# Kernel optimization log

Measured on AMD Instinct MI355X. Metric: run time of the kernel, lower is better.

Reference implementation:

```python
import jax, jax.numpy as jnp
import numpy as np

N, E, G = 50000, 600000, 500          # nodes, edges, graphs in batch
IN_NODE, HID, EDGE = 92, 64, 41       # CGCNN default feature dims
NCONV, PRED, NOUT = 3, 128, 1
Z_DIM = 2 * HID + EDGE                # 169: cat(src_x, dst_x, edge_attr)
BN_EPS = 1e-5


def setup_inputs() -> dict:
    key = jax.random.key(0)
    ks = jax.random.split(key, 14)
    f32 = jnp.float32
    return {
        "x": jax.random.normal(ks[0], (N, IN_NODE), f32),
        "edge_attr": jax.random.normal(ks[1], (E, EDGE), f32),
        "src": jax.random.randint(ks[2], (E,), 0, N),
        "dst": jax.random.randint(ks[3], (E,), 0, N),
        "graph_idx": jnp.sort(jax.random.randint(ks[4], (N,), 0, G)),
        "n_graphs": G,
        "W_embed": jax.random.normal(ks[5], (IN_NODE, HID), f32) / np.sqrt(IN_NODE),
        "b_embed": jnp.zeros((HID,), f32),
        "W_sig": jax.random.normal(ks[6], (NCONV, Z_DIM, HID), f32) / np.sqrt(Z_DIM),
        "b_sig": jnp.zeros((NCONV, HID), f32),
        "W_sp": jax.random.normal(ks[7], (NCONV, Z_DIM, HID), f32) / np.sqrt(Z_DIM),
        "b_sp": jnp.zeros((NCONV, HID), f32),
        "bn_gamma": jnp.ones((NCONV, HID), f32),
        "bn_beta": jnp.zeros((NCONV, HID), f32),
        "W_fc": jax.random.normal(ks[8], (HID, PRED), f32) / np.sqrt(HID),
        "b_fc": jnp.zeros((PRED,), f32),
        "W_out": jax.random.normal(ks[9], (PRED, NOUT), f32) / np.sqrt(PRED),
        "b_out": jnp.zeros((NOUT,), f32),
    }


def reference(x, edge_attr, src, dst, graph_idx, n_graphs,
              W_embed, b_embed, W_sig, b_sig, W_sp, b_sp,
              bn_gamma, bn_beta, W_fc, b_fc, W_out, b_out):
    # node embedding to hidden dim
    h = x @ W_embed + b_embed                                   # [N, HID]
    n_nodes = h.shape[0]
    for i in range(W_sig.shape[0]):
        # per-edge features: gather src/dst node feats + edge feats
        z = jnp.concatenate([h[src], h[dst], edge_attr], axis=1)  # [E, Z_DIM]
        gated = jax.nn.sigmoid(z @ W_sig[i] + b_sig[i])           # [E, HID]
        msg = jax.nn.softplus(z @ W_sp[i] + b_sp[i])              # [E, HID]
        # scatter-sum gated messages into destination node mailboxes
        agg = jax.ops.segment_sum(gated * msg, dst, num_segments=n_nodes)
        h = h + agg                                               # residual
        # batch norm over nodes (training-mode batch stats, biased var)
        mean = h.mean(axis=0)
        var = h.var(axis=0)
        h = (h - mean) * jax.lax.rsqrt(var + BN_EPS) * bn_gamma[i] + bn_beta[i]
    # sum-pool nodes per graph, then dense readout
    graph_feat = jax.ops.segment_sum(h, graph_idx, num_segments=n_graphs)  # [G, HID]
    graph_feat = graph_feat @ W_fc + b_fc                                  # [G, PRED]
    return graph_feat @ W_out + b_out                                      # [G, NOUT]
```

## Files before the change

### kernel.cpp

```cpp
#include <hip/hip_runtime.h>

#define N_NODES 50000
#define N_EDGES 600000
#define N_GRAPHS 500
#define IN_F 92
#define HID 64
#define EDGE_F 41
#define ZDIM 169
#define PRED 128
#define BN_EPS 1e-5f
#define SCAN_BLOCKS 196
#define ROW_U32 24
#define LOG2E 1.4426950408889634f
#define LN2   0.6931471805599453f

typedef unsigned int u32;
typedef _Float16 f16;
typedef _Float16 f16x2 __attribute__((ext_vector_type(2)));
typedef _Float16 f16x8 __attribute__((ext_vector_type(8)));
typedef float f32x4 __attribute__((ext_vector_type(4)));

__device__ __forceinline__ u32 f2bf(float f) {
    u32 u = __float_as_uint(f);
    return (u + 0x7fffu + ((u >> 16) & 1u)) >> 16;
}

__device__ __forceinline__ int lbound(const int* __restrict__ a, int nelem, int val) {
    int lo = 0, hi = nelem;
    while (lo < hi) {
        int m = (lo + hi) >> 1;
        if (a[m] < val) lo = m + 1; else hi = m;
    }
    return lo;
}

__global__ void k_zeroAll(int* __restrict__ ip, int n1, float* __restrict__ fp, int n2) {
    int i = blockIdx.x * 256 + threadIdx.x;
    if (i < n1) ip[i] = 0;
    else if (i - n1 < n2) fp[i - n1] = 0.f;
}

__global__ void k_hist(const int* __restrict__ dst, int* __restrict__ deg) {
    int e = blockIdx.x * 256 + threadIdx.x;
    if (e < N_EDGES) atomicAdd(&deg[dst[e]], 1);
}

__global__ __launch_bounds__(256) void k_scanA(const int* __restrict__ deg,
                                               int* __restrict__ partial) {
    __shared__ int s[256];
    int i = blockIdx.x * 256 + threadIdx.x;
    s[threadIdx.x] = (i < N_NODES) ? deg[i] : 0;
    __syncthreads();
    for (int off = 128; off > 0; off >>= 1) {
        if (threadIdx.x < off) s[threadIdx.x] += s[threadIdx.x + off];
        __syncthreads();
    }
    if (threadIdx.x == 0) partial[blockIdx.x] = s[0];
}

__global__ __launch_bounds__(256) void k_scanB(const int* __restrict__ partial,
                                               int* __restrict__ partialExc,
                                               int* __restrict__ rowptr) {
    __shared__ int s[256];
    int t = threadIdx.x;
    int v = (t < SCAN_BLOCKS) ? partial[t] : 0;
    s[t] = v;
    __syncthreads();
    for (int off = 1; off < 256; off <<= 1) {
        int x = (t >= off) ? s[t - off] : 0;
        __syncthreads();
        s[t] += x;
        __syncthreads();
    }
    partialExc[t] = s[t] - v;
    if (t == 0) rowptr[N_NODES] = N_EDGES;
}

__global__ __launch_bounds__(256) void k_scanC(const int* __restrict__ deg,
                                               const int* __restrict__ partialExc,
                                               int* __restrict__ rowptr) {
    __shared__ int s[256];
    int i = blockIdx.x * 256 + threadIdx.x;
    int t = threadIdx.x;
    int v = (i < N_NODES) ? deg[i] : 0;
    s[t] = v;
    __syncthreads();
    for (int off = 1; off < 256; off <<= 1) {
        int x = (t >= off) ? s[t - off] : 0;
        __syncthreads();
        s[t] += x;
        __syncthreads();
    }
    if (i < N_NODES) rowptr[i] = s[t] - v + partialExc[blockIdx.x];
}

__global__ void k_rank(const int* __restrict__ dst, const int* __restrict__ src,
                       const int* __restrict__ rowptr, int* __restrict__ cursor,
                       int* __restrict__ srcS, int* __restrict__ iperm) {
    int e = blockIdx.x * 256 + threadIdx.x;
    if (e >= N_EDGES) {
        if (e < N_EDGES + 32) srcS[e] = 0;
        return;
    }
    int d = dst[e];
    int p = rowptr[d] + atomicAdd(&cursor[d], 1);
    srcS[p] = src[e];
    iperm[p] = e;
}

__global__ __launch_bounds__(256) void k_epackS(const float* __restrict__ ea,
                                                const int* __restrict__ iperm,
                                                u32* __restrict__ eapS) {
    const int total = N_EDGES * ROW_U32;
    const int stride = gridDim.x * 256;
    for (int idx = blockIdx.x * 256 + threadIdx.x; idx < total; idx += stride) {
        int p = idx / ROW_U32;
        int q = idx - p * ROW_U32;
        int e = iperm[p];
        int k0 = 2 * q, k1 = k0 + 1;
        float f0 = (k0 < EDGE_F) ? ea[(size_t)e * EDGE_F + k0] : 0.f;
        float f1 = (k1 < EDGE_F) ? ea[(size_t)e * EDGE_F + k1] : 0.f;
        f16x2 hv = {(f16)f0, (f16)f1};
        eapS[idx] = __builtin_bit_cast(u32, hv);
    }
}

__global__ void k_wprepAll(const float* __restrict__ Wsig, const float* __restrict__ Wsp,
                           const float* __restrict__ Wemb,
                           f16* __restrict__ Wf16, f16* __restrict__ Wp2,
                           f16* __restrict__ Wef) {
    int t = blockIdx.x * 256 + threadIdx.x;
    if (t < 3072) {
        int lane = t & 63;
        int jt = (t >> 6) & 7;
        int kt = (t >> 9) & 1;
        int L = t >> 10;
        int j128 = jt * 16 + (lane & 15);
        const float* Wbase = (j128 < 64) ? Wsig : Wsp;
        int j = j128 & 63;
        f16x8 v;
        #pragma unroll
        for (int b = 0; b < 8; ++b) {
            int k = kt * 32 + (lane >> 4) * 8 + b;
            float f = (k < EDGE_F) ? Wbase[(size_t)L * ZDIM * HID + (128 + k) * HID + j] * LOG2E : 0.f;
            v[b] = (f16)f;
        }
        *(f16x8*)(Wf16 + ((size_t)((L * 2 + kt) * 8 + jt) * 64 + lane) * 8) = v;
    } else if (t < 9216) {
        int t2 = t - 3072;
        int lane = t2 & 63;
        int jt = (t2 >> 6) & 15;
        int kt = (t2 >> 10) & 1;
        int L = t2 >> 11;
        int j256 = jt * 16 + (lane & 15);
        const float* Wbase = (j256 & 64) ? Wsp : Wsig;
        int rowoff = (j256 & 128) ? 64 : 0;
        int j = j256 & 63;
        f16x8 v;
        #pragma unroll
        for (int b = 0; b < 8; ++b) {
            int k = kt * 32 + (lane >> 4) * 8 + b;
            v[b] = (f16)Wbase[(size_t)L * ZDIM * HID + (rowoff + k) * HID + j];
        }
        *(f16x8*)(Wp2 + ((size_t)((L * 2 + kt) * 16 + jt) * 64 + lane) * 8) = v;
    } else if (t < 9984) {
        int t3 = t - 9216;
        int lane = t3 & 63;
        int jt = (t3 >> 6) & 3;
        int kt = t3 >> 8;
        int j = jt * 16 + (lane & 15);
        f16x8 v;
        #pragma unroll
        for (int b = 0; b < 8; ++b) {
            int k = kt * 32 + (lane >> 4) * 8 + b;
            v[b] = (k < IN_F) ? (f16)Wemb[(size_t)k * HID + j] : (f16)0.f;
        }
        *(f16x8*)(Wef + ((size_t)(kt * 4 + jt) * 64 + lane) * 8) = v;
    }
}

__global__ __launch_bounds__(256) void k_embedm(const float* __restrict__ x,
                                                const f16* __restrict__ Wef,
                                                const float* __restrict__ b,
                                                float* __restrict__ A) {
    __shared__ f16x8 Wl[12 * 64];
    for (int i = threadIdx.x; i < 12 * 64; i += 256) Wl[i] = ((const f16x8*)Wef)[i];
    __syncthreads();
    const int lane = threadIdx.x & 63;
    const int col = lane & 15, grp = lane >> 4;
    float bj[4];
    #pragma unroll
    for (int jt = 0; jt < 4; ++jt) bj[jt] = b[jt * 16 + col];
    const int wid = blockIdx.x * 4 + (threadIdx.x >> 6);
    const int nw = gridDim.x * 4;
    for (int c = wid; c < N_NODES / 16; c += nw) {
        const int node = c * 16 + col;
        const float* xr = x + (size_t)node * IN_F;
        f16x8 af[3];
        #pragma unroll
        for (int kt = 0; kt < 3; ++kt) {
            int base = kt * 32 + grp * 8;
            float4 v0 = *(const float4*)(xr + base);
            float4 v1 = (base + 4 < IN_F) ? *(const float4*)(xr + base + 4)
                                          : make_float4(0.f, 0.f, 0.f, 0.f);
            af[kt] = f16x8{(f16)v0.x, (f16)v0.y, (f16)v0.z, (f16)v0.w,
                           (f16)v1.x, (f16)v1.y, (f16)v1.z, (f16)v1.w};
        }
        #pragma unroll
        for (int jt = 0; jt < 4; ++jt) {
            f32x4 c4 = {};
            c4 = __builtin_amdgcn_mfma_f32_16x16x32_f16(af[0], Wl[(0 * 4 + jt) * 64 + lane], c4, 0, 0, 0);
            c4 = __builtin_amdgcn_mfma_f32_16x16x32_f16(af[1], Wl[(1 * 4 + jt) * 64 + lane], c4, 0, 0, 0);
            c4 = __builtin_amdgcn_mfma_f32_16x16x32_f16(af[2], Wl[(2 * 4 + jt) * 64 + lane], c4, 0, 0, 0);
            #pragma unroll
            for (int r = 0; r < 4; ++r)
                A[(size_t)(c * 16 + grp * 4 + r) * HID + jt * 16 + col] = c4[r] + bj[jt];
        }
    }
}

__global__ __launch_bounds__(256, 4) void k_projm(const float* __restrict__ A,
                                                  const float* __restrict__ statsPrev,
                                                  const float* __restrict__ gammaP,
                                                  const float* __restrict__ betaP,
                                                  int applyBN,
                                                  const f16* __restrict__ Wp2L,
                                                  const float* __restrict__ bsig,
                                                  const float* __restrict__ bsp,
                                                  u32* __restrict__ pA,
                                                  u32* __restrict__ pB,
                                                  float* __restrict__ statsOut) {
    __shared__ f16x8 Wl[32 * 64];
    for (int i = threadIdx.x; i < 32 * 64; i += 256) Wl[i] = ((const f16x8*)Wp2L)[i];
    if (blockIdx.x == 0)
        for (int i = threadIdx.x; i < 128 * 32; i += 256) statsOut[i] = 0.f;
    __syncthreads();
    const int lane = threadIdx.x & 63;
    const int col = lane & 15;
    float sck[2][8], shk[2][8];
    #pragma unroll
    for (int kt = 0; kt < 2; ++kt)
        #pragma unroll
        for (int b = 0; b < 8; ++b) {
            int k = kt * 32 + (lane >> 4) * 8 + b;
            float scv = 1.f, shv = 0.f;
            if (applyBN) {
                float m = statsPrev[k * 32] * (1.f / N_NODES);
                float v = statsPrev[(64 + k) * 32] * (1.f / N_NODES) - m * m;
                scv = rsqrtf(v + BN_EPS) * gammaP[k];
                shv = betaP[k] - m * scv;
            }
            sck[kt][b] = scv;
            shk[kt][b] = shv;
        }
    float bAs[4], bPs[4];
    #pragma unroll
    for (int jt = 0; jt < 4; ++jt) {
        bAs[jt] = bsig[jt * 16 + col] * LOG2E;
        bPs[jt] = bsp[jt * 16 + col] * LOG2E;
    }
    const int wid = blockIdx.x * 4 + (threadIdx.x >> 6);
    const int nw = gridDim.x * 4;
    for (int c = wid; c < N_NODES / 16; c += nw) {
        const int node = c * 16 + col;
        const float4* Arow = (const float4*)(A + (size_t)node * HID);
        f16x8 af[2];
        #pragma unroll
        for (int kt = 0; kt < 2; ++kt) {
            float4 v0 = Arow[kt * 8 + (lane >> 4) * 2];
            float4 v1 = Arow[kt * 8 + (lane >> 4) * 2 + 1];
            float e0 = v0.x * sck[kt][0] + shk[kt][0];
            float e1 = v0.y * sck[kt][1] + shk[kt][1];
            float e2 = v0.z * sck[kt][2] + shk[kt][2];
            float e3 = v0.w * sck[kt][3] + shk[kt][3];
            float e4 = v1.x * sck[kt][4] + shk[kt][4];
            float e5 = v1.y * sck[kt][5] + shk[kt][5];
            float e6 = v1.z * sck[kt][6] + shk[kt][6];
            float e7 = v1.w * sck[kt][7] + shk[kt][7];
            af[kt] = f16x8{(f16)e0, (f16)e1, (f16)e2, (f16)e3,
                           (f16)e4, (f16)e5, (f16)e6, (f16)e7};
        }
        #pragma unroll
        for (int h = 0; h < 2; ++h) {
            f32x4 c4[8];
            #pragma unroll
            for (int jt2 = 0; jt2 < 8; ++jt2) {
                int jt = h * 8 + jt2;
                f32x4 acc = {};
                acc = __builtin_amdgcn_mfma_f32_16x16x32_f16(af[0], Wl[(0 * 16 + jt) * 64 + lane], acc, 0, 0, 0);
                c4[jt2] = __builtin_amdgcn_mfma_f32_16x16x32_f16(af[1], Wl[(1 * 16 + jt) * 64 + lane], acc, 0, 0, 0);
            }
            u32* dstArr = h ? pB : pA;
            #pragma unroll
            for (int jt2 = 0; jt2 < 4; ++jt2)
                #pragma unroll
                for (int r = 0; r < 4; ++r) {
                    float s = fmaf(c4[jt2][r], LOG2E, h ? 0.f : bAs[jt2]);
                    float p = fmaf(c4[jt2 + 4][r], LOG2E, h ? 0.f : bPs[jt2]);
                    int n2 = c * 16 + (lane >> 4) * 4 + r;
                    dstArr[(size_t)n2 * HID + jt2 * 16 + col] = f2bf(s) | (f2bf(p) << 16);
                }
        }
    }
}

__global__ __launch_bounds__(256) void k_nodeagg(const float* __restrict__ A,
                                                 const float* __restrict__ statsPrev,
                                                 const float* __restrict__ gammaP,
                                                 const float* __restrict__ betaP,
                                                 int applyBN,
                                                 const u32* __restrict__ pAv,
                                                 const u32* __restrict__ pBv,
                                                 const u32* __restrict__ eapS,
                                                 const int* __restrict__ srcS,
                                                 const int* __restrict__ rowptr,
                                                 const f16* __restrict__ Wf16L,
                                                 float* __restrict__ Aout,
                                                 float* __restrict__ statsOut) {
    const int lane = threadIdx.x & 63;
    const int col = lane & 15;
    const int grp = lane >> 4;
    const int rowb = grp * 4;

    const f16x8* WfL = (const f16x8*)Wf16L;
    f16x8 bfrag[2][8];
    #pragma unroll
    for (int kt = 0; kt < 2; ++kt)
        #pragma unroll
        for (int jt = 0; jt < 8; ++jt)
            bfrag[kt][jt] = WfL[(kt * 8 + jt) * 64 + lane];

    float scL = 1.f, shL = 0.f;
    if (applyBN) {
        float m = statsPrev[lane * 32] * (1.f / N_NODES);
        float v = statsPrev[(64 + lane) * 32] * (1.f / N_NODES) - m * m;
        scL = rsqrtf(v + BN_EPS) * gammaP[lane];
        shL = betaP[lane] - m * scL;
    }

    const int nwaves = gridDim.x << 2;
    const int w = (blockIdx.x << 2) + (threadIdx.x >> 6);
    const int T = (N_EDGES + 1 + nwaves - 1) / nwaves;
    int nb = min(lbound(rowptr, N_NODES + 1, w * T), N_NODES);
    int ne = min(lbound(rowptr, N_NODES + 1, w * T + T), N_NODES);

    float lsum = 0.f, lsq = 0.f;
    if (nb < ne) {
        int rb = rowptr[nb];
        int re = rowptr[nb + 1];
        float resid = A[(size_t)nb * HID + lane];
        if (applyBN) resid = resid * scL + shL;
        u32 pb4[4];
        #pragma unroll
        for (int jt = 0; jt < 4; ++jt) pb4[jt] = pBv[(size_t)nb * HID + jt * 16 + col];
        int s0 = srcS[rb + rowb + 0], s1 = srcS[rb + rowb + 1],
            s2 = srcS[rb + rowb + 2], s3 = srcS[rb + rowb + 3];

        for (int n = nb; n < ne; ++n) {
            const int nn = (n + 1 < N_NODES) ? n + 1 : n;
            const int re_nx = rowptr[nn + 1];
            float resid_nx = A[(size_t)nn * HID + lane];
            if (applyBN) resid_nx = resid_nx * scL + shL;
            u32 pbx[4];
            #pragma unroll
            for (int jt = 0; jt < 4; ++jt) pbx[jt] = pBv[(size_t)nn * HID + jt * 16 + col];

            float bsigj[4], bspj[4];
            #pragma unroll
            for (int jt = 0; jt < 4; ++jt) {
                bsigj[jt] = __uint_as_float(pb4[jt] << 16);
                bspj[jt]  = __uint_as_float(pb4[jt] & 0xffff0000u);
            }
            float accv[4] = {0.f, 0.f, 0.f, 0.f};
            for (int et = rb; et < re; et += 16) {
                const int cnt = re - et;
                u32 ga[4][4];
                #pragma unroll
                for (int jt = 0; jt < 4; ++jt) {
                    ga[jt][0] = pAv[(size_t)s0 * HID + jt * 16 + col];
                    ga[jt][1] = pAv[(size_t)s1 * HID + jt * 16 + col];
                    ga[jt][2] = pAv[(size_t)s2 * HID + jt * 16 + col];
                    ga[jt][3] = pAv[(size_t)s3 * HID + jt * 16 + col];
                }
                const f16x8* arow = (const f16x8*)(eapS + (size_t)(et + col) * ROW_U32);
                f16x8 a0 = arow[grp];
                f16x8 a1 = arow[4 + grp];
                const int nxt = (et + 16 < re) ? et + 16 : re;
                const int t0n = srcS[nxt + rowb + 0], t1n = srcS[nxt + rowb + 1],
                          t2n = srcS[nxt + rowb + 2], t3n = srcS[nxt + rowb + 3];
                #pragma unroll
                for (int jt = 0; jt < 4; ++jt) {
                    f32x4 cs = {}, cp = {};
                    cs = __builtin_amdgcn_mfma_f32_16x16x32_f16(a0, bfrag[0][jt], cs, 0, 0, 0);
                    cs = __builtin_amdgcn_mfma_f32_16x16x32_f16(a1, bfrag[1][jt], cs, 0, 0, 0);
                    cp = __builtin_amdgcn_mfma_f32_16x16x32_f16(a0, bfrag[0][jt + 4], cp, 0, 0, 0);
                    cp = __builtin_amdgcn_mfma_f32_16x16x32_f16(a1, bfrag[1][jt + 4], cp, 0, 0, 0);
                    #pragma unroll
                    for (int r = 0; r < 4; ++r) {
                        float s_ = cs[r] + __uint_as_float(ga[jt][r] << 16) + bsigj[jt];
                        float p_ = cp[r] + __uint_as_float(ga[jt][r] & 0xffff0000u) + bspj[jt];
                        float g_ = __builtin_amdgcn_rcpf(1.f + exp2f(-s_));
                        float m_ = fmaxf(p_, 0.f) + log2f(1.f + exp2f(-fabsf(p_)));
                        accv[jt] += (rowb + r < cnt) ? g_ * m_ : 0.f;
                    }
                }
                s0 = t0n; s1 = t1n; s2 = t2n; s3 = t3n;
            }
            #pragma unroll
            for (int jt = 0; jt < 4; ++jt) {
                accv[jt] += __shfl_xor(accv[jt], 16);
                accv[jt] += __shfl_xor(accv[jt], 32);
            }
            float accSel = (lane & 32) ? ((lane & 16) ? accv[3] : accv[2])
                                       : ((lane & 16) ? accv[1] : accv[0]);
            float outv = resid + accSel * LN2;
            Aout[(size_t)n * HID + lane] = outv;
            lsum += outv;
            lsq += outv * outv;
            rb = re; re = re_nx; resid = resid_nx;
            pb4[0] = pbx[0]; pb4[1] = pbx[1]; pb4[2] = pbx[2]; pb4[3] = pbx[3];
        }
    }

    __shared__ float redS[256], redQ[256];
    redS[threadIdx.x] = lsum;
    redQ[threadIdx.x] = lsq;
    __syncthreads();
    if (threadIdx.x < 64) {
        float s = redS[threadIdx.x] + redS[threadIdx.x + 64] + redS[threadIdx.x + 128] + redS[threadIdx.x + 192];
        float q = redQ[threadIdx.x] + redQ[threadIdx.x + 64] + redQ[threadIdx.x + 128] + redQ[threadIdx.x + 192];
        unsafeAtomicAdd(&statsOut[threadIdx.x * 32], s);
        unsafeAtomicAdd(&statsOut[(64 + threadIdx.x) * 32], q);
    }
}

__global__ __launch_bounds__(256) void k_poolbn(const float* __restrict__ A,
                                                const float* __restrict__ stats,
                                                const float* __restrict__ gamma,
                                                const float* __restrict__ beta,
                                                const int* __restrict__ gidx,
                                                float* __restrict__ gf) {
    const int lane = threadIdx.x & 63;
    float m = stats[lane * 32] * (1.f / N_NODES);
    float v = stats[(64 + lane) * 32] * (1.f / N_NODES) - m * m;
    float scv = rsqrtf(v + BN_EPS) * gamma[lane];
    float shv = beta[lane] - m * scv;
    const int wid = blockIdx.x * 4 + (threadIdx.x >> 6);
    const int nwaves = gridDim.x * 4;
    const int chunk = (N_NODES + nwaves - 1) / nwaves;
    int r0 = wid * chunk;
    if (r0 >= N_NODES) return;
    int r1 = min(r0 + chunk, N_NODES);
    int gcur = gidx[r0];
    float acc = 0.f;
    for (int r = r0; r < r1; ++r) {
        int g = gidx[r];
        if (g != gcur) {
            unsafeAtomicAdd(&gf[(size_t)gcur * HID + lane], acc);
            acc = 0.f;
            gcur = g;
        }
        acc += A[(size_t)r * HID + lane] * scv + shv;
    }
    unsafeAtomicAdd(&gf[(size_t)gcur * HID + lane], acc);
}

__global__ __launch_bounds__(256) void k_readout(const float* __restrict__ gf,
                                                 const float* __restrict__ Wfc,
                                                 const float* __restrict__ bfc,
                                                 const float* __restrict__ Wout,
                                                 const float* __restrict__ bout,
                                                 float* __restrict__ out) {
    const int lane = threadIdx.x & 63;
    const int g = blockIdx.x * 4 + (threadIdx.x >> 6);
    if (g >= N_GRAPHS) return;
    const float* row = gf + (size_t)g * HID;
    float p0 = bfc[lane], p1 = bfc[64 + lane];
    #pragma unroll 4
    for (int k = 0; k < HID; ++k) {
        float v = row[k];
        p0 += v * Wfc[k * PRED + lane];
        p1 += v * Wfc[k * PRED + 64 + lane];
    }
    float part = p0 * Wout[lane] + p1 * Wout[64 + lane];
    #pragma unroll
    for (int off = 32; off > 0; off >>= 1) part += __shfl_xor(part, off);
    if (lane == 0) out[g] = part + bout[0];
}

extern "C" void kernel_launch(void* const* d_in, const int* in_sizes, int n_in,
                              void* d_out, int out_size, void* d_ws, size_t ws_size,
                              hipStream_t stream) {
    const float* x         = (const float*)d_in[0];
    const float* edge_attr = (const float*)d_in[1];
    const int*   src       = (const int*)d_in[2];
    const int*   dst       = (const int*)d_in[3];
    const int*   gidx      = (const int*)d_in[4];
    const float* W_embed   = (const float*)d_in[6];
    const float* b_embed   = (const float*)d_in[7];
    const float* W_sig     = (const float*)d_in[8];
    const float* b_sig     = (const float*)d_in[9];
    const float* W_sp      = (const float*)d_in[10];
    const float* b_sp      = (const float*)d_in[11];
    const float* bn_gamma  = (const float*)d_in[12];
    const float* bn_beta   = (const float*)d_in[13];
    const float* W_fc      = (const float*)d_in[14];
    const float* b_fc      = (const float*)d_in[15];
    const float* W_out     = (const float*)d_in[16];
    const float* b_out     = (const float*)d_in[17];
    float* out = (float*)d_out;

    const size_t NH = (size_t)N_NODES * HID;
    float* ws     = (float*)d_ws;
    float* A      = ws;
    u32*   pA     = (u32*)(A + NH);
    u32*   pB     = pA + NH;
    u32*   eapS   = pB + NH;
    int*   srcS   = (int*)(eapS + (size_t)(N_EDGES + 32) * ROW_U32);
    int*   iperm  = srcS + N_EDGES + 32;
    int*   rowptr = iperm + N_EDGES;
    int*   deg    = rowptr + N_NODES + 1;
    int*   cursor = deg + N_NODES;
    int*   partial    = cursor + N_NODES;
    int*   partialExc = partial + 256;
    f16*   Wf16   = (f16*)(partialExc + 256);
    f16*   Wp2    = Wf16 + 3 * 2 * 8 * 64 * 8;
    f16*   Wef    = Wp2 + 3 * 2 * 16 * 64 * 8;
    float* stats  = (float*)(Wef + 3 * 4 * 64 * 8);
    float* gf     = stats + 3 * 4096;

    k_wprepAll<<<39, 256, 0, stream>>>(W_sig, W_sp, W_embed, Wf16, Wp2, Wef);
    k_zeroAll<<<(2 * N_NODES + N_GRAPHS * HID + 255) / 256, 256, 0, stream>>>(
        deg, 2 * N_NODES, gf, N_GRAPHS * HID);
    k_hist<<<(N_EDGES + 255) / 256, 256, 0, stream>>>(dst, deg);
    k_scanA<<<SCAN_BLOCKS, 256, 0, stream>>>(deg, partial);
    k_scanB<<<1, 256, 0, stream>>>(partial, partialExc, rowptr);
    k_scanC<<<SCAN_BLOCKS, 256, 0, stream>>>(deg, partialExc, rowptr);
    k_rank<<<(N_EDGES + 32 + 255) / 256, 256, 0, stream>>>(dst, src, rowptr, cursor, srcS, iperm);
    k_embedm<<<512, 256, 0, stream>>>(x, Wef, b_embed, A);
    k_epackS<<<4096, 256, 0, stream>>>(edge_attr, iperm, eapS);

    for (int i = 0; i < 3; ++i) {
        const float* stPrev = stats + (size_t)(i > 0 ? i - 1 : 0) * 4096;
        const float* gP     = bn_gamma + (i > 0 ? i - 1 : 0) * HID;
        const float* bP     = bn_beta + (i > 0 ? i - 1 : 0) * HID;
        float* stOut        = stats + (size_t)i * 4096;
        int applyBN = (i > 0) ? 1 : 0;
        k_projm<<<512, 256, 0, stream>>>(A, stPrev, gP, bP, applyBN,
                                         Wp2 + (size_t)i * 2 * 16 * 64 * 8,
                                         b_sig + i * HID, b_sp + i * HID,
                                         pA, pB, stOut);
        k_nodeagg<<<2048, 256, 0, stream>>>(A, stPrev, gP, bP, applyBN,
                                            pA, pB, eapS, srcS, rowptr,
                                            Wf16 + (size_t)i * 2 * 8 * 64 * 8,
                                            A, stOut);
    }

    k_poolbn<<<256, 256, 0, stream>>>(A, stats + 2 * 4096, bn_gamma + 2 * HID,
                                      bn_beta + 2 * HID, gidx, gf);
    k_readout<<<(N_GRAPHS + 3) / 4, 256, 0, stream>>>(gf, W_fc, b_fc, W_out, b_out, out);
}
```

Baseline: 554.2 us.

## Interleave two node-range contexts per wave in edge aggregation kernel

After: 528.9 us. 1.05x faster.

```diff
diff --git a/kernel.cpp b/kernel.cpp
--- a/kernel.cpp
+++ b/kernel.cpp
@@ -13,6 +13,9 @@
 #define ROW_U32 24
 #define LOG2E 1.4426950408889634f
 #define LN2   0.6931471805599453f
+#define NAGG_BLOCKS 2048
+#define NW2 (NAGG_BLOCKS * 8)
+#define PART_T ((N_EDGES + 1 + NW2 - 1) / NW2)
 
 typedef unsigned int u32;
 typedef _Float16 f16;
@@ -92,6 +95,11 @@
         __syncthreads();
     }
     if (i < N_NODES) rowptr[i] = s[t] - v + partialExc[blockIdx.x];
+}
+
+__global__ void k_part(const int* __restrict__ rowptr, int* __restrict__ partW) {
+    int i = blockIdx.x * 256 + threadIdx.x;
+    if (i <= NW2) partW[i] = min(lbound(rowptr, N_NODES + 1, i * PART_T), N_NODES);
 }
 
 __global__ void k_rank(const int* __restrict__ dst, const int* __restrict__ src,
@@ -304,31 +312,139 @@
     }
 }
 
-__global__ __launch_bounds__(256) void k_nodeagg(const float* __restrict__ A,
-                                                 const float* __restrict__ statsPrev,
-                                                 const float* __restrict__ gammaP,
-                                                 const float* __restrict__ betaP,
-                                                 int applyBN,
-                                                 const u32* __restrict__ pAv,
-                                                 const u32* __restrict__ pBv,
-                                                 const u32* __restrict__ eapS,
-                                                 const int* __restrict__ srcS,
-                                                 const int* __restrict__ rowptr,
-                                                 const f16* __restrict__ Wf16L,
-                                                 float* __restrict__ Aout,
-                                                 float* __restrict__ statsOut) {
+
+#define CTX_DECL_INIT(S, widx)                                                \
+    int n##S = __builtin_amdgcn_readfirstlane(partW[widx]);                   \
+    const int ne##S = __builtin_amdgcn_readfirstlane(partW[(widx) + 1]);      \
+    bool act##S = n##S < ne##S;                                               \
+    int rb##S = 0, re##S = 0;                                                 \
+    float resid##S = 0.f;                                                     \
+    float bsg##S[4], bsp##S[4], accv##S[4];                                   \
+    int s0##S = 0, s1##S = 0, s2##S = 0, s3##S = 0;                           \
+    {                                                                         \
+        _Pragma("unroll")                                                     \
+        for (int jt = 0; jt < 4; ++jt) {                                      \
+            bsg##S[jt] = 0.f; bsp##S[jt] = 0.f; accv##S[jt] = 0.f;            \
+        }                                                                     \
+        if (act##S) {                                                         \
+            rb##S = __builtin_amdgcn_readfirstlane(rowptr[n##S]);             \
+            re##S = __builtin_amdgcn_readfirstlane(rowptr[n##S + 1]);         \
+            resid##S = A[(size_t)n##S * HID + lane];                          \
+            if (applyBN) resid##S = resid##S * scL + shL;                     \
+            _Pragma("unroll")                                                 \
+            for (int jt = 0; jt < 4; ++jt) {                                  \
+                u32 pb = pBv[(size_t)n##S * HID + jt * 16 + col];             \
+                bsg##S[jt] = __uint_as_float(pb << 16);                       \
+                bsp##S[jt] = __uint_as_float(pb & 0xffff0000u);               \
+            }                                                                 \
+            const int* sp = srcS + rb##S + rowb;                              \
+            s0##S = sp[0]; s1##S = sp[1]; s2##S = sp[2]; s3##S = sp[3];       \
+        }                                                                     \
+    }
+
+#define STEP_LOADS(S)                                                         \
+    u32 ga##S[4][4];                                                          \
+    f16x8 a0##S, a1##S;                                                       \
+    if (act##S) {                                                             \
+        const u32* g0##S = pAv + (size_t)s0##S * HID + col;                   \
+        const u32* g1##S = pAv + (size_t)s1##S * HID + col;                   \
+        const u32* g2##S = pAv + (size_t)s2##S * HID + col;                   \
+        const u32* g3##S = pAv + (size_t)s3##S * HID + col;                   \
+        _Pragma("unroll")                                                     \
+        for (int jt = 0; jt < 4; ++jt) {                                      \
+            ga##S[jt][0] = g0##S[jt * 16];                                    \
+            ga##S[jt][1] = g1##S[jt * 16];                                    \
+            ga##S[jt][2] = g2##S[jt * 16];                                    \
+            ga##S[jt][3] = g3##S[jt * 16];                                    \
+        }                                                                     \
+        const f16x8* arow##S = (const f16x8*)(eapS + (size_t)(rb##S + col) * ROW_U32); \
+        a0##S = arow##S[grp];                                                 \
+        a1##S = arow##S[4 + grp];                                             \
+    }
+
+#define STEP_COMPUTE(S)                                                       \
+    if (act##S) {                                                             \
+        const int cnt##S = re##S - rb##S;                                     \
+        if (cnt##S > 0) {                                                     \
+            _Pragma("unroll")                                                 \
+            for (int jt = 0; jt < 4; ++jt) {                                  \
+                f32x4 cs = {bsg##S[jt], bsg##S[jt], bsg##S[jt], bsg##S[jt]};  \
+                f32x4 cp = {bsp##S[jt], bsp##S[jt], bsp##S[jt], bsp##S[jt]};  \
+                f16x8 w0s = Wlds[(jt) * 64 + lane];                           \
+                f16x8 w1s = Wlds[(8 + jt) * 64 + lane];                       \
+                f16x8 w0p = Wlds[(4 + jt) * 64 + lane];                       \
+                f16x8 w1p = Wlds[(12 + jt) * 64 + lane];                      \
+                cs = __builtin_amdgcn_mfma_f32_16x16x32_f16(a0##S, w0s, cs, 0, 0, 0); \
+                cs = __builtin_amdgcn_mfma_f32_16x16x32_f16(a1##S, w1s, cs, 0, 0, 0); \
+                cp = __builtin_amdgcn_mfma_f32_16x16x32_f16(a0##S, w0p, cp, 0, 0, 0); \
+                cp = __builtin_amdgcn_mfma_f32_16x16x32_f16(a1##S, w1p, cp, 0, 0, 0); \
+                _Pragma("unroll")                                             \
+                for (int r = 0; r < 4; ++r) {                                 \
+                    float s_ = cs[r] + __uint_as_float(ga##S[jt][r] << 16);   \
+                    float p_ = cp[r] + __uint_as_float(ga##S[jt][r] & 0xffff0000u); \
+                    float g_ = __builtin_amdgcn_rcpf(1.f + exp2f(-s_));       \
+                    float m_ = fmaxf(p_, 0.f) + log2f(1.f + exp2f(-fabsf(p_))); \
+                    accv##S[jt] += (rowb + r < cnt##S) ? g_ * m_ : 0.f;       \
+                }                                                             \
+            }                                                                 \
+            rb##S += 16;                                                      \
+        }                                                                     \
+        while (rb##S >= re##S) {                                              \
+            _Pragma("unroll")                                                 \
+            for (int jt = 0; jt < 4; ++jt) {                                  \
+                accv##S[jt] += __shfl_xor(accv##S[jt], 16);                   \
+                accv##S[jt] += __shfl_xor(accv##S[jt], 32);                   \
+            }                                                                 \
+            float accSel = (lane & 32) ? ((lane & 16) ? accv##S[3] : accv##S[2]) \
+                                       : ((lane & 16) ? accv##S[1] : accv##S[0]); \
+            float outv = resid##S + accSel * LN2;                             \
+            Aout[(size_t)n##S * HID + lane] = outv;                           \
+            lsum += outv;                                                     \
+            lsq += outv * outv;                                               \
+            accv##S[0] = accv##S[1] = accv##S[2] = accv##S[3] = 0.f;          \
+            rb##S = re##S;                                                    \
+            ++n##S;                                                           \
+            if (n##S >= ne##S) { act##S = false; break; }                     \
+            re##S = __builtin_amdgcn_readfirstlane(rowptr[n##S + 1]);         \
+            resid##S = A[(size_t)n##S * HID + lane];                          \
+            if (applyBN) resid##S = resid##S * scL + shL;                     \
+            _Pragma("unroll")                                                 \
+            for (int jt = 0; jt < 4; ++jt) {                                  \
+                u32 pb = pBv[(size_t)n##S * HID + jt * 16 + col];             \
+                bsg##S[jt] = __uint_as_float(pb << 16);                       \
+                bsp##S[jt] = __uint_as_float(pb & 0xffff0000u);               \
+            }                                                                 \
+        }                                                                     \
+        if (act##S) {                                                         \
+            const int* sp##S = srcS + rb##S + rowb;                           \
+            s0##S = sp##S[0]; s1##S = sp##S[1];                               \
+            s2##S = sp##S[2]; s3##S = sp##S[3];                               \
+        }                                                                     \
+    }
+
+__global__ __launch_bounds__(256, 4) void k_nodeagg(const float* __restrict__ A,
+                                                    const float* __restrict__ statsPrev,
+                                                    const float* __restrict__ gammaP,
+                                                    const float* __restrict__ betaP,
+                                                    int applyBN,
+                                                    const u32* __restrict__ pAv,
+                                                    const u32* __restrict__ pBv,
+                                                    const u32* __restrict__ eapS,
+                                                    const int* __restrict__ srcS,
+                                                    const int* __restrict__ rowptr,
+                                                    const int* __restrict__ partW,
+                                                    const f16* __restrict__ Wf16L,
+                                                    float* __restrict__ Aout,
+                                                    float* __restrict__ statsOut) {
+    __shared__ f16x8 Wlds[16 * 64];
+    __shared__ float redS[256], redQ[256];
+    for (int i = threadIdx.x; i < 16 * 64; i += 256)
+        Wlds[i] = ((const f16x8*)Wf16L)[i];
+
     const int lane = threadIdx.x & 63;
     const int col = lane & 15;
     const int grp = lane >> 4;
     const int rowb = grp * 4;
-
-    const f16x8* WfL = (const f16x8*)Wf16L;
-    f16x8 bfrag[2][8];
-    #pragma unroll
-    for (int kt = 0; kt < 2; ++kt)
-        #pragma unroll
-        for (int jt = 0; jt < 8; ++jt)
-            bfrag[kt][jt] = WfL[(kt * 8 + jt) * 64 + lane];
 
     float scL = 1.f, shL = 0.f;
     if (applyBN) {
@@ -337,92 +453,21 @@
         scL = rsqrtf(v + BN_EPS) * gammaP[lane];
         shL = betaP[lane] - m * scL;
     }
-
-    const int nwaves = gridDim.x << 2;
-    const int w = (blockIdx.x << 2) + (threadIdx.x >> 6);
-    const int T = (N_EDGES + 1 + nwaves - 1) / nwaves;
-    int nb = min(lbound(rowptr, N_NODES + 1, w * T), N_NODES);
-    int ne = min(lbound(rowptr, N_NODES + 1, w * T + T), N_NODES);
-
+    __syncthreads();
+
+    const int w2 = (((blockIdx.x << 2) + (threadIdx.x >> 6)) << 1);
     float lsum = 0.f, lsq = 0.f;
-    if (nb < ne) {
-        int rb = rowptr[nb];
-        int re = rowptr[nb + 1];
-        float resid = A[(size_t)nb * HID + lane];
-        if (applyBN) resid = resid * scL + shL;
-        u32 pb4[4];
-        #pragma unroll
-        for (int jt = 0; jt < 4; ++jt) pb4[jt] = pBv[(size_t)nb * HID + jt * 16 + col];
-        int s0 = srcS[rb + rowb + 0], s1 = srcS[rb + rowb + 1],
-            s2 = srcS[rb + rowb + 2], s3 = srcS[rb + rowb + 3];
-
-        for (int n = nb; n < ne; ++n) {
-            const int nn = (n + 1 < N_NODES) ? n + 1 : n;
-            const int re_nx = rowptr[nn + 1];
-            float resid_nx = A[(size_t)nn * HID + lane];
-            if (applyBN) resid_nx = resid_nx * scL + shL;
-            u32 pbx[4];
-            #pragma unroll
-            for (int jt = 0; jt < 4; ++jt) pbx[jt] = pBv[(size_t)nn * HID + jt * 16 + col];
-
-            float bsigj[4], bspj[4];
-            #pragma unroll
-            for (int jt = 0; jt < 4; ++jt) {
-                bsigj[jt] = __uint_as_float(pb4[jt] << 16);
-                bspj[jt]  = __uint_as_float(pb4[jt] & 0xffff0000u);
-            }
-            float accv[4] = {0.f, 0.f, 0.f, 0.f};
-            for (int et = rb; et < re; et += 16) {
-                const int cnt = re - et;
-                u32 ga[4][4];
-                #pragma unroll
-                for (int jt = 0; jt < 4; ++jt) {
-                    ga[jt][0] = pAv[(size_t)s0 * HID + jt * 16 + col];
-                    ga[jt][1] = pAv[(size_t)s1 * HID + jt * 16 + col];
-                    ga[jt][2] = pAv[(size_t)s2 * HID + jt * 16 + col];
-                    ga[jt][3] = pAv[(size_t)s3 * HID + jt * 16 + col];
-                }
-                const f16x8* arow = (const f16x8*)(eapS + (size_t)(et + col) * ROW_U32);
-                f16x8 a0 = arow[grp];
-                f16x8 a1 = arow[4 + grp];
-                const int nxt = (et + 16 < re) ? et + 16 : re;
-                const int t0n = srcS[nxt + rowb + 0], t1n = srcS[nxt + rowb + 1],
-                          t2n = srcS[nxt + rowb + 2], t3n = srcS[nxt + rowb + 3];
-                #pragma unroll
-                for (int jt = 0; jt < 4; ++jt) {
-                    f32x4 cs = {}, cp = {};
-                    cs = __builtin_amdgcn_mfma_f32_16x16x32_f16(a0, bfrag[0][jt], cs, 0, 0, 0);
-                    cs = __builtin_amdgcn_mfma_f32_16x16x32_f16(a1, bfrag[1][jt], cs, 0, 0, 0);
-                    cp = __builtin_amdgcn_mfma_f32_16x16x32_f16(a0, bfrag[0][jt + 4], cp, 0, 0, 0);
-                    cp = __builtin_amdgcn_mfma_f32_16x16x32_f16(a1, bfrag[1][jt + 4], cp, 0, 0, 0);
-                    #pragma unroll
-                    for (int r = 0; r < 4; ++r) {
-                        float s_ = cs[r] + __uint_as_float(ga[jt][r] << 16) + bsigj[jt];
-                        float p_ = cp[r] + __uint_as_float(ga[jt][r] & 0xffff0000u) + bspj[jt];
-                        float g_ = __builtin_amdgcn_rcpf(1.f + exp2f(-s_));
-                        float m_ = fmaxf(p_, 0.f) + log2f(1.f + exp2f(-fabsf(p_)));
-                        accv[jt] += (rowb + r < cnt) ? g_ * m_ : 0.f;
-                    }
-                }
-                s0 = t0n; s1 = t1n; s2 = t2n; s3 = t3n;
-            }
-            #pragma unroll
-            for (int jt = 0; jt < 4; ++jt) {
-                accv[jt] += __shfl_xor(accv[jt], 16);
-                accv[jt] += __shfl_xor(accv[jt], 32);
-            }
-            float accSel = (lane & 32) ? ((lane & 16) ? accv[3] : accv[2])
-                                       : ((lane & 16) ? accv[1] : accv[0]);
-            float outv = resid + accSel * LN2;
-            Aout[(size_t)n * HID + lane] = outv;
-            lsum += outv;
-            lsq += outv * outv;
-            rb = re; re = re_nx; resid = resid_nx;
-            pb4[0] = pbx[0]; pb4[1] = pbx[1]; pb4[2] = pbx[2]; pb4[3] = pbx[3];
-        }
-    }
-
-    __shared__ float redS[256], redQ[256];
+
+    CTX_DECL_INIT(A, w2)
+    CTX_DECL_INIT(B, w2 + 1)
+
+    while (actA || actB) {
+        STEP_LOADS(A)
+        STEP_LOADS(B)
+        STEP_COMPUTE(A)
+        STEP_COMPUTE(B)
+    }
+
     redS[threadIdx.x] = lsum;
     redQ[threadIdx.x] = lsq;
     __syncthreads();
@@ -523,7 +568,8 @@
     int*   cursor = deg + N_NODES;
     int*   partial    = cursor + N_NODES;
     int*   partialExc = partial + 256;
-    f16*   Wf16   = (f16*)(partialExc + 256);
+    int*   partW  = partialExc + 256;
+    f16*   Wf16   = (f16*)(partW + NW2 + 2);
     f16*   Wp2    = Wf16 + 3 * 2 * 8 * 64 * 8;
     f16*   Wef    = Wp2 + 3 * 2 * 16 * 64 * 8;
     float* stats  = (float*)(Wef + 3 * 4 * 64 * 8);
@@ -536,6 +582,7 @@
     k_scanA<<<SCAN_BLOCKS, 256, 0, stream>>>(deg, partial);
     k_scanB<<<1, 256, 0, stream>>>(partial, partialExc, rowptr);
     k_scanC<<<SCAN_BLOCKS, 256, 0, stream>>>(deg, partialExc, rowptr);
+    k_part<<<(NW2 + 1 + 255) / 256, 256, 0, stream>>>(rowptr, partW);
     k_rank<<<(N_EDGES + 32 + 255) / 256, 256, 0, stream>>>(dst, src, rowptr, cursor, srcS, iperm);
     k_embedm<<<512, 256, 0, stream>>>(x, Wef, b_embed, A);
     k_epackS<<<4096, 256, 0, stream>>>(edge_attr, iperm, eapS);
@@ -550,10 +597,10 @@
                                          Wp2 + (size_t)i * 2 * 16 * 64 * 8,
                                          b_sig + i * HID, b_sp + i * HID,
                                          pA, pB, stOut);
-        k_nodeagg<<<2048, 256, 0, stream>>>(A, stPrev, gP, bP, applyBN,
-                                            pA, pB, eapS, srcS, rowptr,
-                                            Wf16 + (size_t)i * 2 * 8 * 64 * 8,
-                                            A, stOut);
+        k_nodeagg<<<NAGG_BLOCKS, 256, 0, stream>>>(A, stPrev, gP, bP, applyBN,
+                                                   pA, pB, eapS, srcS, rowptr, partW,
+                                                   Wf16 + (size_t)i * 2 * 8 * 64 * 8,
+                                                   A, stOut);
     }
 
     k_poolbn<<<256, 256, 0, stream>>>(A, stats + 2 * 4096, bn_gamma + 2 * HID,
```
